# Optimization experiments

Hardware: AMD Instinct MI355X
Metric: run time of the kernel (lower is better)

Reference implementation:

```python
import jax, jax.numpy as jnp
import numpy as np

N_NODES = 100000
N_EDGES = 600000
DIMS = [128, 64, 32, 2]


def gcn_conv(x, edge_index, W, b, n_nodes):
    """PyG GCNConv (eval mode): symmetric-normalized aggregation with self-loops.
    out = D^{-1/2} (A + I) D^{-1/2} (x W) + b
    """
    h = x @ W  # [N, out] -- transform first (cheaper when out < in)
    src = jnp.concatenate([edge_index[0], jnp.arange(n_nodes)])  # add self-loops
    dst = jnp.concatenate([edge_index[1], jnp.arange(n_nodes)])
    deg = jax.ops.segment_sum(jnp.ones_like(dst, dtype=h.dtype), dst,
                              num_segments=n_nodes)  # in-degree incl. self-loop
    dinv = jax.lax.rsqrt(deg)
    norm = dinv[src] * dinv[dst]  # [E+N]
    msg = norm[:, None] * h[src]  # gather + scale
    out = jax.ops.segment_sum(msg, dst, num_segments=n_nodes)  # scatter-add
    return out + b


def setup_inputs() -> dict:
    key = jax.random.key(0)
    ks = jax.random.split(key, 8)
    x = jax.random.normal(ks[0], (N_NODES, DIMS[0]), dtype=jnp.float32)
    edge_index = jax.random.randint(ks[1], (2, N_EDGES), 0, N_NODES, dtype=jnp.int64)
    inp = {"x": x, "edge_index": edge_index}
    for i in range(3):
        fan_in, fan_out = DIMS[i], DIMS[i + 1]
        s = 1.0 / np.sqrt(fan_in)
        inp[f"W{i+1}"] = jax.random.uniform(ks[2 + 2 * i], (fan_in, fan_out),
                                            minval=-s, maxval=s, dtype=jnp.float32)
        inp[f"b{i+1}"] = jnp.zeros((fan_out,), dtype=jnp.float32)
    return inp


def reference(x, edge_index, W1, b1, W2, b2, W3, b3):
    # 3 stacked GCNConv layers with ReLU; dropout is identity in eval mode.
    n = x.shape[0]
    x = jax.nn.relu(gcn_conv(x, edge_index, W1, b1, n))
    x = jax.nn.relu(gcn_conv(x, edge_index, W2, b2, n))
    x = jax.nn.relu(gcn_conv(x, edge_index, W3, b3, n))
    return x
```

## Files before the change

kernel.cpp:

```cpp
#include <hip/hip_runtime.h>
#include <math.h>


#define FULL_GRID 2048
#define PARTS 8

typedef const __attribute__((address_space(1))) void* gas_ptr;
typedef __attribute__((address_space(3))) void* las_ptr;

__device__ __forceinline__ void gld16(const void* g, void* l) {
  __builtin_amdgcn_global_load_lds((gas_ptr)g, (las_ptr)l, 16, 0, 0);
}

__global__ __launch_bounds__(256) void k_init(int* __restrict__ p, int n4,
                                              const unsigned int* __restrict__ words,
                                              int* __restrict__ flag) {
  if (blockIdx.x == gridDim.x - 1) {
    __shared__ int sm[256];
    int cnt = 0;
    #pragma unroll
    for (int j = 0; j < 8; ++j) {
      int idx = (threadIdx.x * 8 + j) * 2 + 1;
      cnt += (words[idx] == 0u) ? 1 : 0;
    }
    sm[threadIdx.x] = cnt;
    __syncthreads();
    for (int off = 128; off > 0; off >>= 1) {
      if (threadIdx.x < off) sm[threadIdx.x] += sm[threadIdx.x + off];
      __syncthreads();
    }
    if (threadIdx.x == 0) flag[0] = (sm[0] > 1024) ? 1 : 0;
    return;
  }
  int i = blockIdx.x * blockDim.x + threadIdx.x;
  const int stride = (gridDim.x - 1) * blockDim.x;
  int4* p4 = (int4*)p;
  for (; i < n4; i += stride) p4[i] = make_int4(0, 0, 0, 0);
}

__global__ __launch_bounds__(256) void k_hist(const void* __restrict__ eraw, int E,
                                              int N, const int* __restrict__ flag,
                                              int* __restrict__ counts) {
  const int is64 = flag[0];
  const int part = blockIdx.x & (PARTS - 1);
  const int lo = (int)((long long)N * part / PARTS);
  const int hi = (int)((long long)N * (part + 1) / PARTS);
  int i = (blockIdx.x >> 3) * blockDim.x + threadIdx.x;
  const int stride = (gridDim.x >> 3) * blockDim.x;
  if (is64) {
    const long long* e = (const long long*)eraw;
    for (; i < E; i += stride) {
      const int d = (int)e[(long long)E + i];
      if (d >= lo && d < hi) atomicAdd(&counts[d], 1);
    }
  } else {
    const int* e = (const int*)eraw;
    for (; i < E; i += stride) {
      const int d = e[E + i];
      if (d >= lo && d < hi) atomicAdd(&counts[d], 1);
    }
  }
}

__global__ __launch_bounds__(1024) void k_scan1(const int* __restrict__ counts,
                                                int* __restrict__ scanned,
                                                int* __restrict__ partials, int n) {
  __shared__ int sm[1024];
  const int i = blockIdx.x * 1024 + threadIdx.x;
  const int v = (i < n) ? counts[i] : 0;
  sm[threadIdx.x] = v;
  __syncthreads();
  for (int off = 1; off < 1024; off <<= 1) {
    int t = sm[threadIdx.x];
    int u = (threadIdx.x >= off) ? sm[threadIdx.x - off] : 0;
    __syncthreads();
    sm[threadIdx.x] = t + u;
    __syncthreads();
  }
  const int inc = sm[threadIdx.x];
  if (i < n) scanned[i] = inc - v;
  if (threadIdx.x == 1023) partials[blockIdx.x] = inc;
}

__global__ __launch_bounds__(256) void k_scan3(const int* __restrict__ scanned,
                                               const int* __restrict__ partials,
                                               int nb,
                                               const int* __restrict__ counts,
                                               int* __restrict__ offsets,
                                               int* __restrict__ cursor,
                                               float* __restrict__ dinv, int n) {
  __shared__ int ps[1024];
  for (int t = threadIdx.x; t < nb; t += 256) ps[t] = partials[t];
  __syncthreads();
  if (threadIdx.x == 0) {
    int run = 0;
    for (int b = 0; b < nb; ++b) { const int v = ps[b]; ps[b] = run; run += v; }
  }
  __syncthreads();
  int i = blockIdx.x * blockDim.x + threadIdx.x;
  const int stride = gridDim.x * blockDim.x;
  for (; i < n; i += stride) {
    const int o = scanned[i] + ps[i >> 10];
    offsets[i] = o;
    cursor[i] = o;
    dinv[i] = rsqrtf((float)counts[i] + 1.0f);
  }
}

__global__ __launch_bounds__(256) void k_fill(const void* __restrict__ eraw, int E,
                                              int N, const int* __restrict__ flag,
                                              int* __restrict__ cursor,
                                              int* __restrict__ elist) {
  const int is64 = flag[0];
  const int part = blockIdx.x & (PARTS - 1);
  const int lo = (int)((long long)N * part / PARTS);
  const int hi = (int)((long long)N * (part + 1) / PARTS);
  int i = (blockIdx.x >> 3) * blockDim.x + threadIdx.x;
  const int stride = (gridDim.x >> 3) * blockDim.x;
  if (is64) {
    const long long* e = (const long long*)eraw;
    for (; i < E; i += stride) {
      const int d = (int)e[(long long)E + i];
      if (d >= lo && d < hi) {
        const int s = (int)e[i];
        elist[atomicAdd(&cursor[d], 1)] = s;
      }
    }
  } else {
    const int* e = (const int*)eraw;
    for (; i < E; i += stride) {
      const int d = e[E + i];
      if (d >= lo && d < hi) {
        const int s = e[i];
        elist[atomicAdd(&cursor[d], 1)] = s;
      }
    }
  }
}

template <int F_IN, int F_OUT, int TILE_M, int KC>
__global__ __launch_bounds__(256) void k_transform(const float* __restrict__ X,
                                                   const float* __restrict__ W,
                                                   const float* __restrict__ dinv,
                                                   float* __restrict__ H, int n) {
  constexpr int COLT = F_OUT / 4;
  constexpr int ROWT = 256 / COLT;
  constexpr int TM = TILE_M / ROWT;
  constexpr int NKC = F_IN / KC;
  constexpr int K4 = F_IN / 4;
  constexpr int NWB = (NKC > 1) ? 2 : 1;
  static_assert(TM * ROWT == TILE_M && COLT * 4 == F_OUT, "tiling");
  static_assert((TILE_M * F_IN * 4) % 1024 == 0 && (KC * F_OUT * 4) % 1024 == 0, "segs");
  static_assert(K4 >= 8, "swizzle range");
  static_assert(ROWT % 8 == 0, "swizzle invariance across r");

  __shared__ __align__(16) float Xs[TILE_M * F_IN];
  __shared__ __align__(16) float Ws[NWB][KC * F_OUT];

  const int tid = threadIdx.x;
  const int lane = tid & 63;
  const int wid = tid >> 6;
  const long long base = (long long)blockIdx.x * TILE_M;

  const float4* __restrict__ X4 = (const float4*)X;
  if (base + TILE_M <= n) {
    constexpr int SEGS = TILE_M * F_IN * 4 / 1024;
    constexpr int PW = SEGS / 4;
    #pragma unroll
    for (int j = 0; j < PW; ++j) {
      const int seg = wid * PW + j;
      const int slot = seg * 64 + lane;
      const int row = slot / K4;
      const int c = slot % K4;
      const int ksrc = c ^ (row & 7);
      gld16(&X4[(base + row) * K4 + ksrc], &Xs[seg * 256]);
    }
  } else {
    for (int slot = tid; slot < TILE_M * K4; slot += 256) {
      const int row = slot / K4;
      const int c = slot % K4;
      float4 v = make_float4(0.f, 0.f, 0.f, 0.f);
      if (base + row < n) v = X4[(base + row) * K4 + (c ^ (row & 7))];
      ((float4*)Xs)[slot] = v;
    }
  }

  constexpr int WSEG = KC * F_OUT * 4 / 1024;
  constexpr int WPW = WSEG / 4;
  {
    #pragma unroll
    for (int j = 0; j < WPW; ++j) {
      const int seg = wid * WPW + j;
      gld16(W + seg * 256 + lane * 4, &Ws[0][seg * 256]);
    }
  }

  const int ct = tid % COLT;
  const int rt = tid / COLT;
  const int sw = rt & 7;

  float4 acc[TM];
  #pragma unroll
  for (int r = 0; r < TM; ++r) acc[r] = make_float4(0.f, 0.f, 0.f, 0.f);

  const float4* Xs4 = (const float4*)Xs;

  for (int kc = 0; kc < NKC; ++kc) {
    __syncthreads();
    if (NKC > 1 && kc + 1 < NKC) {
      const float* wb = W + (kc + 1) * KC * F_OUT;
      #pragma unroll
      for (int j = 0; j < WPW; ++j) {
        const int seg = wid * WPW + j;
        gld16(wb + seg * 256 + lane * 4, &Ws[(kc + 1) & (NWB - 1)][seg * 256]);
      }
    }
    const float4* Ws4 = (const float4*)Ws[kc & (NWB - 1)];
    #pragma unroll
    for (int k4 = 0; k4 < KC / 4; ++k4) {
      const int kk = kc * (KC / 4) + k4;
      float4 wv0 = Ws4[(k4 * 4 + 0) * COLT + ct];
      float4 wv1 = Ws4[(k4 * 4 + 1) * COLT + ct];
      float4 wv2 = Ws4[(k4 * 4 + 2) * COLT + ct];
      float4 wv3 = Ws4[(k4 * 4 + 3) * COLT + ct];
      #pragma unroll
      for (int r = 0; r < TM; ++r) {
        const float4 xv = Xs4[(rt + r * ROWT) * K4 + (kk ^ sw)];
        acc[r].x = fmaf(xv.x, wv0.x, acc[r].x);
        acc[r].y = fmaf(xv.x, wv0.y, acc[r].y);
        acc[r].z = fmaf(xv.x, wv0.z, acc[r].z);
        acc[r].w = fmaf(xv.x, wv0.w, acc[r].w);
        acc[r].x = fmaf(xv.y, wv1.x, acc[r].x);
        acc[r].y = fmaf(xv.y, wv1.y, acc[r].y);
        acc[r].z = fmaf(xv.y, wv1.z, acc[r].z);
        acc[r].w = fmaf(xv.y, wv1.w, acc[r].w);
        acc[r].x = fmaf(xv.z, wv2.x, acc[r].x);
        acc[r].y = fmaf(xv.z, wv2.y, acc[r].y);
        acc[r].z = fmaf(xv.z, wv2.z, acc[r].z);
        acc[r].w = fmaf(xv.z, wv2.w, acc[r].w);
        acc[r].x = fmaf(xv.w, wv3.x, acc[r].x);
        acc[r].y = fmaf(xv.w, wv3.y, acc[r].y);
        acc[r].z = fmaf(xv.w, wv3.z, acc[r].z);
        acc[r].w = fmaf(xv.w, wv3.w, acc[r].w);
      }
    }
  }

  #pragma unroll
  for (int r = 0; r < TM; ++r) {
    const long long row = base + rt + r * ROWT;
    if (row < n) {
      const float di = dinv[row];
      float4 v = acc[r];
      v.x *= di; v.y *= di; v.z *= di; v.w *= di;
      *(float4*)&H[row * F_OUT + ct * 4] = v;
    }
  }
}

template <int F, bool RELU_OUT, bool FUSE_W3>
__global__ __launch_bounds__(256) void k_agg_vec(const float* __restrict__ HS,
                                                 const float* __restrict__ dinv,
                                                 const int* __restrict__ offsets,
                                                 const int* __restrict__ counts,
                                                 const int* __restrict__ elist,
                                                 const float* __restrict__ bias,
                                                 const float* __restrict__ W3,
                                                 float* __restrict__ out, int n) {
  constexpr int LPE = F / 4;
  constexpr int EPW = 64 / LPE;
  const int lane = threadIdx.x & 63;
  const int wv = (blockIdx.x * (blockDim.x >> 6)) + (threadIdx.x >> 6);
  const int nwaves = gridDim.x * (blockDim.x >> 6);
  const int g = lane / LPE;
  const int fl = lane % LPE;
  const float4 bf = *(const float4*)&bias[fl * 4];

  float w3a0 = 0.f, w3a1 = 0.f, w3a2 = 0.f, w3a3 = 0.f;
  float w3b0 = 0.f, w3b1 = 0.f, w3b2 = 0.f, w3b3 = 0.f;
  if (FUSE_W3) {
    w3a0 = W3[(fl * 4 + 0) * 2 + 0]; w3b0 = W3[(fl * 4 + 0) * 2 + 1];
    w3a1 = W3[(fl * 4 + 1) * 2 + 0]; w3b1 = W3[(fl * 4 + 1) * 2 + 1];
    w3a2 = W3[(fl * 4 + 2) * 2 + 0]; w3b2 = W3[(fl * 4 + 2) * 2 + 1];
    w3a3 = W3[(fl * 4 + 3) * 2 + 0]; w3b3 = W3[(fl * 4 + 3) * 2 + 1];
  }

  for (long long d = wv; d < n; d += nwaves) {
    const float di = dinv[d];
    const int start = offsets[d];
    const int cnt = counts[d];
    float4 acc = make_float4(0.f, 0.f, 0.f, 0.f);
    if (g == 0) acc = *(const float4*)&HS[d * F + fl * 4];

    for (int j = 0; j < cnt; j += 2 * EPW) {
      const int e0 = j + g;
      const int e1 = j + EPW + g;
      const int i0 = elist[start + (e0 < cnt ? e0 : cnt - 1)];
      const int i1 = elist[start + (e1 < cnt ? e1 : cnt - 1)];
      const float4 v0 = *(const float4*)&HS[(long long)i0 * F + fl * 4];
      const float4 v1 = *(const float4*)&HS[(long long)i1 * F + fl * 4];
      if (e0 < cnt) {
        acc.x += v0.x; acc.y += v0.y; acc.z += v0.z; acc.w += v0.w;
      }
      if (e1 < cnt) {
        acc.x += v1.x; acc.y += v1.y; acc.z += v1.z; acc.w += v1.w;
      }
    }
    #pragma unroll
    for (int m = LPE; m < 64; m <<= 1) {
      acc.x += __shfl_xor(acc.x, m, 64);
      acc.y += __shfl_xor(acc.y, m, 64);
      acc.z += __shfl_xor(acc.z, m, 64);
      acc.w += __shfl_xor(acc.w, m, 64);
    }
    float4 r;
    r.x = fmaf(di, acc.x, bf.x);
    r.y = fmaf(di, acc.y, bf.y);
    r.z = fmaf(di, acc.z, bf.z);
    r.w = fmaf(di, acc.w, bf.w);
    if (RELU_OUT) {
      r.x = fmaxf(r.x, 0.f); r.y = fmaxf(r.y, 0.f);
      r.z = fmaxf(r.z, 0.f); r.w = fmaxf(r.w, 0.f);
    }
    if (!FUSE_W3) {
      if (g == 0) *(float4*)&out[d * F + fl * 4] = r;
    } else {
      float t0 = r.x * w3a0 + r.y * w3a1 + r.z * w3a2 + r.w * w3a3;
      float t1 = r.x * w3b0 + r.y * w3b1 + r.z * w3b2 + r.w * w3b3;
      #pragma unroll
      for (int m = 1; m < LPE; m <<= 1) {
        t0 += __shfl_xor(t0, m, 64);
        t1 += __shfl_xor(t1, m, 64);
      }
      if (lane == 0) {
        out[d * 2 + 0] = di * t0;
        out[d * 2 + 1] = di * t1;
      }
    }
  }
}

template <int F, bool RELU_OUT>
__global__ __launch_bounds__(256) void k_aggregate(const float* __restrict__ HS,
                                                   const float* __restrict__ dinv,
                                                   const int* __restrict__ offsets,
                                                   const int* __restrict__ counts,
                                                   const int* __restrict__ elist,
                                                   const float* __restrict__ bias,
                                                   float* __restrict__ out, int n) {
  const int f = threadIdx.x % F;
  const int grp = threadIdx.x / F;
  constexpr int GRPS = 256 / F;
  const float bf = bias[f];

  for (long long d = (long long)blockIdx.x * GRPS + grp; d < n;
       d += (long long)gridDim.x * GRPS) {
    const float di = dinv[d];
    float acc = HS[d * F + f];
    const int start = offsets[d];
    const int cnt = counts[d];
    for (int j = 0; j < cnt; j += 8) {
      int idx[8];
      float v[8];
      #pragma unroll
      for (int t = 0; t < 8; ++t) {
        const int jj = (j + t < cnt) ? (j + t) : j;
        idx[t] = elist[start + jj];
      }
      #pragma unroll
      for (int t = 0; t < 8; ++t) v[t] = HS[(long long)idx[t] * F + f];
      #pragma unroll
      for (int t = 0; t < 8; ++t) acc += (j + t < cnt) ? v[t] : 0.f;
    }
    float r = fmaf(di, acc, bf);
    if (RELU_OUT) r = fmaxf(r, 0.f);
    out[d * F + f] = r;
  }
}

extern "C" void kernel_launch(void* const* d_in, const int* in_sizes, int n_in,
                              void* d_out, int out_size, void* d_ws, size_t ws_size,
                              hipStream_t stream) {
  const float* x = (const float*)d_in[0];
  const void* eraw = d_in[1];
  const float* W1 = (const float*)d_in[2];
  const float* b1 = (const float*)d_in[3];
  const float* W2 = (const float*)d_in[4];
  const float* b2 = (const float*)d_in[5];
  const float* W3 = (const float*)d_in[6];
  const float* b3 = (const float*)d_in[7];
  float* out = (float*)d_out;

  const int N = in_sizes[0] / 128;
  const int E = in_sizes[1] / 2;

  char* ws = (char*)d_ws;
  size_t off = 0;
  auto alloc = [&](size_t bytes) -> char* {
    char* p = ws + off;
    off = (off + bytes + 255) & ~(size_t)255;
    return p;
  };
  int*   flag     = (int*)alloc(256);
  int*   counts   = (int*)alloc((size_t)N * 4 + 16);
  int*   scanned  = (int*)alloc((size_t)N * 4);
  int*   partials = (int*)alloc(1024 * 4);
  int*   offsets  = (int*)alloc((size_t)N * 4);
  int*   cursor   = (int*)alloc((size_t)N * 4);
  int*   elist    = (int*)alloc((size_t)E * 4);
  float* dinv     = (float*)alloc((size_t)N * 4);
  float* hbuf     = (float*)alloc((size_t)N * 64 * 4);
  float* obuf     = (float*)alloc((size_t)N * 64 * 4);
  float* h2buf    = (float*)alloc((size_t)N * 32 * 4);
  (void)ws_size; (void)n_in; (void)out_size;

  k_init<<<129, 256, 0, stream>>>(counts, (N + 3) / 4, (const unsigned int*)eraw,
                                  flag);
  k_hist<<<FULL_GRID, 256, 0, stream>>>(eraw, E, N, flag, counts);
  const int NB = (N + 1023) >> 10;
  k_scan1<<<NB, 1024, 0, stream>>>(counts, scanned, partials, N);
  k_scan3<<<(N + 255) / 256, 256, 0, stream>>>(scanned, partials, NB, counts,
                                               offsets, cursor, dinv, N);
  k_fill<<<FULL_GRID, 256, 0, stream>>>(eraw, E, N, flag, cursor, elist);

  k_transform<128, 64, 64, 16><<<(N + 63) / 64, 256, 0, stream>>>(x, W1, dinv, hbuf, N);
  k_agg_vec<64, true, false><<<FULL_GRID, 256, 0, stream>>>(
      hbuf, dinv, offsets, counts, elist, b1, nullptr, obuf, N);

  k_transform<64, 32, 128, 64><<<(N + 127) / 128, 256, 0, stream>>>(obuf, W2, dinv,
                                                                    h2buf, N);
  k_agg_vec<32, true, true><<<FULL_GRID, 256, 0, stream>>>(
      h2buf, dinv, offsets, counts, elist, b2, W3, hbuf, N);

  k_aggregate<2, true><<<(N + 127) / 128, 256, 0, stream>>>(
      hbuf, dinv, offsets, counts, elist, b3, out, N);
}
```

Measured before the change: 194.2 us.

## Shrink transform blocks to one wave with 8x8 per-thread register tiles

The dense transform kernel now launches single-wave (64-thread) blocks in place of 256-thread ones. Each thread accumulates an 8-row by 8-column register tile, so every LDS weight and X read feeds more FMAs. The second layer also uses smaller double-buffered K chunks. The trade-off is that each block still holds the same large X tile in LDS, so the CU can host far fewer resident waves, which weakens latency hiding for the global-to-LDS loads.

```diff
diff --git a/kernel.cpp b/kernel.cpp
--- a/kernel.cpp
+++ b/kernel.cpp
@@ -138,45 +138,45 @@
   }
 }
 
-template <int F_IN, int F_OUT, int TILE_M, int KC>
-__global__ __launch_bounds__(256) void k_transform(const float* __restrict__ X,
-                                                   const float* __restrict__ W,
-                                                   const float* __restrict__ dinv,
-                                                   float* __restrict__ H, int n) {
-  constexpr int COLT = F_OUT / 4;
-  constexpr int ROWT = 256 / COLT;
-  constexpr int TM = TILE_M / ROWT;
+__device__ __forceinline__ float f4get(const float4& v, int j) {
+  return j == 0 ? v.x : (j == 1 ? v.y : (j == 2 ? v.z : v.w));
+}
+
+template <int F_IN, int F_OUT, int KC>
+__global__ __launch_bounds__(64) void k_transform(const float* __restrict__ X,
+                                                  const float* __restrict__ W,
+                                                  const float* __restrict__ dinv,
+                                                  float* __restrict__ H, int n) {
+  constexpr int COLT = F_OUT / 8;
+  constexpr int ROWT = 64 / COLT;
+  constexpr int TILE_M = 8 * ROWT;
+  constexpr int K4 = F_IN / 4;
   constexpr int NKC = F_IN / KC;
-  constexpr int K4 = F_IN / 4;
   constexpr int NWB = (NKC > 1) ? 2 : 1;
-  static_assert(TM * ROWT == TILE_M && COLT * 4 == F_OUT, "tiling");
-  static_assert((TILE_M * F_IN * 4) % 1024 == 0 && (KC * F_OUT * 4) % 1024 == 0, "segs");
-  static_assert(K4 >= 8, "swizzle range");
-  static_assert(ROWT % 8 == 0, "swizzle invariance across r");
+  constexpr int F4 = F_OUT / 4;
+  static_assert(COLT * 8 == F_OUT && ROWT * COLT == 64, "tiling");
+  static_assert(K4 >= 8 && (ROWT % 8) == 0, "swizzle");
+  static_assert((TILE_M * F_IN * 4) % 1024 == 0, "X segs");
+  static_assert((KC * F_OUT * 4) % 1024 == 0, "W segs");
 
   __shared__ __align__(16) float Xs[TILE_M * F_IN];
   __shared__ __align__(16) float Ws[NWB][KC * F_OUT];
 
-  const int tid = threadIdx.x;
-  const int lane = tid & 63;
-  const int wid = tid >> 6;
+  const int lane = threadIdx.x;
   const long long base = (long long)blockIdx.x * TILE_M;
-
   const float4* __restrict__ X4 = (const float4*)X;
+
+  constexpr int XSEG = TILE_M * F_IN * 4 / 1024;
   if (base + TILE_M <= n) {
-    constexpr int SEGS = TILE_M * F_IN * 4 / 1024;
-    constexpr int PW = SEGS / 4;
     #pragma unroll
-    for (int j = 0; j < PW; ++j) {
-      const int seg = wid * PW + j;
-      const int slot = seg * 64 + lane;
+    for (int j = 0; j < XSEG; ++j) {
+      const int slot = j * 64 + lane;
       const int row = slot / K4;
       const int c = slot % K4;
-      const int ksrc = c ^ (row & 7);
-      gld16(&X4[(base + row) * K4 + ksrc], &Xs[seg * 256]);
+      gld16(&X4[(base + row) * K4 + (c ^ (row & 7))], &Xs[j * 256]);
     }
   } else {
-    for (int slot = tid; slot < TILE_M * K4; slot += 256) {
+    for (int slot = lane; slot < TILE_M * K4; slot += 64) {
       const int row = slot / K4;
       const int c = slot % K4;
       float4 v = make_float4(0.f, 0.f, 0.f, 0.f);
@@ -186,22 +186,19 @@
   }
 
   constexpr int WSEG = KC * F_OUT * 4 / 1024;
-  constexpr int WPW = WSEG / 4;
-  {
-    #pragma unroll
-    for (int j = 0; j < WPW; ++j) {
-      const int seg = wid * WPW + j;
-      gld16(W + seg * 256 + lane * 4, &Ws[0][seg * 256]);
-    }
-  }
-
-  const int ct = tid % COLT;
-  const int rt = tid / COLT;
+  #pragma unroll
+  for (int j = 0; j < WSEG; ++j) gld16(W + j * 256 + lane * 4, &Ws[0][j * 256]);
+
+  const int ct = lane % COLT;
+  const int rt = lane / COLT;
   const int sw = rt & 7;
 
-  float4 acc[TM];
+  float4 acc[8][2];
   #pragma unroll
-  for (int r = 0; r < TM; ++r) acc[r] = make_float4(0.f, 0.f, 0.f, 0.f);
+  for (int r = 0; r < 8; ++r) {
+    acc[r][0] = make_float4(0.f, 0.f, 0.f, 0.f);
+    acc[r][1] = make_float4(0.f, 0.f, 0.f, 0.f);
+  }
 
   const float4* Xs4 = (const float4*)Xs;
 
@@ -210,50 +207,49 @@
     if (NKC > 1 && kc + 1 < NKC) {
       const float* wb = W + (kc + 1) * KC * F_OUT;
       #pragma unroll
-      for (int j = 0; j < WPW; ++j) {
-        const int seg = wid * WPW + j;
-        gld16(wb + seg * 256 + lane * 4, &Ws[(kc + 1) & (NWB - 1)][seg * 256]);
-      }
+      for (int j = 0; j < WSEG; ++j)
+        gld16(wb + j * 256 + lane * 4, &Ws[(kc + 1) & (NWB - 1)][j * 256]);
     }
     const float4* Ws4 = (const float4*)Ws[kc & (NWB - 1)];
     #pragma unroll
-    for (int k4 = 0; k4 < KC / 4; ++k4) {
-      const int kk = kc * (KC / 4) + k4;
-      float4 wv0 = Ws4[(k4 * 4 + 0) * COLT + ct];
-      float4 wv1 = Ws4[(k4 * 4 + 1) * COLT + ct];
-      float4 wv2 = Ws4[(k4 * 4 + 2) * COLT + ct];
-      float4 wv3 = Ws4[(k4 * 4 + 3) * COLT + ct];
-      #pragma unroll
-      for (int r = 0; r < TM; ++r) {
+    for (int lk4 = 0; lk4 < KC / 4; ++lk4) {
+      const int kk = kc * (KC / 4) + lk4;
+      float4 wv[4][2];
+      #pragma unroll
+      for (int j = 0; j < 4; ++j) {
+        wv[j][0] = Ws4[(lk4 * 4 + j) * F4 + 2 * ct + 0];
+        wv[j][1] = Ws4[(lk4 * 4 + j) * F4 + 2 * ct + 1];
+      }
+      #pragma unroll
+      for (int r = 0; r < 8; ++r) {
         const float4 xv = Xs4[(rt + r * ROWT) * K4 + (kk ^ sw)];
-        acc[r].x = fmaf(xv.x, wv0.x, acc[r].x);
-        acc[r].y = fmaf(xv.x, wv0.y, acc[r].y);
-        acc[r].z = fmaf(xv.x, wv0.z, acc[r].z);
-        acc[r].w = fmaf(xv.x, wv0.w, acc[r].w);
-        acc[r].x = fmaf(xv.y, wv1.x, acc[r].x);
-        acc[r].y = fmaf(xv.y, wv1.y, acc[r].y);
-        acc[r].z = fmaf(xv.y, wv1.z, acc[r].z);
-        acc[r].w = fmaf(xv.y, wv1.w, acc[r].w);
-        acc[r].x = fmaf(xv.z, wv2.x, acc[r].x);
-        acc[r].y = fmaf(xv.z, wv2.y, acc[r].y);
-        acc[r].z = fmaf(xv.z, wv2.z, acc[r].z);
-        acc[r].w = fmaf(xv.z, wv2.w, acc[r].w);
-        acc[r].x = fmaf(xv.w, wv3.x, acc[r].x);
-        acc[r].y = fmaf(xv.w, wv3.y, acc[r].y);
-        acc[r].z = fmaf(xv.w, wv3.z, acc[r].z);
-        acc[r].w = fmaf(xv.w, wv3.w, acc[r].w);
+        #pragma unroll
+        for (int j = 0; j < 4; ++j) {
+          const float xs = f4get(xv, j);
+          acc[r][0].x = fmaf(xs, wv[j][0].x, acc[r][0].x);
+          acc[r][0].y = fmaf(xs, wv[j][0].y, acc[r][0].y);
+          acc[r][0].z = fmaf(xs, wv[j][0].z, acc[r][0].z);
+          acc[r][0].w = fmaf(xs, wv[j][0].w, acc[r][0].w);
+          acc[r][1].x = fmaf(xs, wv[j][1].x, acc[r][1].x);
+          acc[r][1].y = fmaf(xs, wv[j][1].y, acc[r][1].y);
+          acc[r][1].z = fmaf(xs, wv[j][1].z, acc[r][1].z);
+          acc[r][1].w = fmaf(xs, wv[j][1].w, acc[r][1].w);
+        }
       }
     }
   }
 
   #pragma unroll
-  for (int r = 0; r < TM; ++r) {
+  for (int r = 0; r < 8; ++r) {
     const long long row = base + rt + r * ROWT;
     if (row < n) {
       const float di = dinv[row];
-      float4 v = acc[r];
-      v.x *= di; v.y *= di; v.z *= di; v.w *= di;
-      *(float4*)&H[row * F_OUT + ct * 4] = v;
+      #pragma unroll
+      for (int c4 = 0; c4 < 2; ++c4) {
+        float4 v = acc[r][c4];
+        v.x *= di; v.y *= di; v.z *= di; v.w *= di;
+        *(float4*)&H[row * F_OUT + ct * 8 + c4 * 4] = v;
+      }
     }
   }
 }
@@ -423,12 +419,12 @@
                                                offsets, cursor, dinv, N);
   k_fill<<<FULL_GRID, 256, 0, stream>>>(eraw, E, N, flag, cursor, elist);
 
-  k_transform<128, 64, 64, 16><<<(N + 63) / 64, 256, 0, stream>>>(x, W1, dinv, hbuf, N);
+  k_transform<128, 64, 16><<<(N + 63) / 64, 64, 0, stream>>>(x, W1, dinv, hbuf, N);
   k_agg_vec<64, true, false><<<FULL_GRID, 256, 0, stream>>>(
       hbuf, dinv, offsets, counts, elist, b1, nullptr, obuf, N);
 
-  k_transform<64, 32, 128, 64><<<(N + 127) / 128, 256, 0, stream>>>(obuf, W2, dinv,
-                                                                    h2buf, N);
+  k_transform<64, 32, 16><<<(N + 127) / 128, 64, 0, stream>>>(obuf, W2, dinv,
+                                                              h2buf, N);
   k_agg_vec<32, true, true><<<FULL_GRID, 256, 0, stream>>>(
       h2buf, dinv, offsets, counts, elist, b2, W3, hbuf, N);
 
```

Result: no change. 196.8 us (+1.3%).

## Use split-bf16 MFMA for the dense layer transforms

Applied to the files above, without the earlier changes.

Replaces the fp32 FMA tiled GEMM for layers 1 and 2 with MFMA 16x16x32 bf16 instructions. Inputs and weights are each split into high and low bf16 parts and combined with three MFMAs to keep near-fp32 accuracy. A small kernel prepacks the weights into fragment layout each call. The goal is to cut the compute time of the transform kernels, at the cost of in-kernel conversion work, extra LDS use, and scalar (non-vector) stores of the output.

```diff
diff --git a/kernel.cpp b/kernel.cpp
--- a/kernel.cpp
+++ b/kernel.cpp
@@ -7,9 +7,20 @@
 
 typedef const __attribute__((address_space(1))) void* gas_ptr;
 typedef __attribute__((address_space(3))) void* las_ptr;
+typedef __attribute__((ext_vector_type(8))) short bf16x8;
+typedef __attribute__((ext_vector_type(4))) float f32x4;
 
 __device__ __forceinline__ void gld16(const void* g, void* l) {
   __builtin_amdgcn_global_load_lds((gas_ptr)g, (las_ptr)l, 16, 0, 0);
+}
+
+__device__ __forceinline__ unsigned short f2bf(float f) {
+  unsigned int u = __float_as_uint(f);
+  u += 0x7FFF + ((u >> 16) & 1);
+  return (unsigned short)(u >> 16);
+}
+__device__ __forceinline__ float bf2f(unsigned short h) {
+  return __uint_as_float(((unsigned int)h) << 16);
 }
 
 __global__ __launch_bounds__(256) void k_init(int* __restrict__ p, int n4,
@@ -36,6 +47,34 @@
   const int stride = (gridDim.x - 1) * blockDim.x;
   int4* p4 = (int4*)p;
   for (; i < n4; i += stride) p4[i] = make_int4(0, 0, 0, 0);
+}
+
+__global__ __launch_bounds__(256) void k_prepw(const float* __restrict__ W1,
+                                               const float* __restrict__ W2,
+                                               short* __restrict__ Wh1,
+                                               short* __restrict__ Wl1,
+                                               short* __restrict__ Wh2,
+                                               short* __restrict__ Wl2) {
+  const int t = blockIdx.x * 256 + threadIdx.x;
+  const int stride = gridDim.x * 256;
+  for (int p = t; p < 4 * 4 * 64 * 8; p += stride) {
+    const int e = p & 7, lane = (p >> 3) & 63, nt = (p >> 9) & 3, kt = p >> 11;
+    const int k = kt * 32 + (lane >> 4) * 8 + e;
+    const int nn = nt * 16 + (lane & 15);
+    const float f = W1[k * 64 + nn];
+    const unsigned short h = f2bf(f);
+    Wh1[p] = (short)h;
+    Wl1[p] = (short)f2bf(f - bf2f(h));
+  }
+  for (int p = t; p < 2 * 2 * 64 * 8; p += stride) {
+    const int e = p & 7, lane = (p >> 3) & 63, nt = (p >> 9) & 1, kt = p >> 10;
+    const int k = kt * 32 + (lane >> 4) * 8 + e;
+    const int nn = nt * 16 + (lane & 15);
+    const float f = W2[k * 32 + nn];
+    const unsigned short h = f2bf(f);
+    Wh2[p] = (short)h;
+    Wl2[p] = (short)f2bf(f - bf2f(h));
+  }
 }
 
 __global__ __launch_bounds__(256) void k_hist(const void* __restrict__ eraw, int E,
@@ -138,122 +177,88 @@
   }
 }
 
-template <int F_IN, int F_OUT, int TILE_M, int KC>
-__global__ __launch_bounds__(256) void k_transform(const float* __restrict__ X,
-                                                   const float* __restrict__ W,
-                                                   const float* __restrict__ dinv,
-                                                   float* __restrict__ H, int n) {
-  constexpr int COLT = F_OUT / 4;
-  constexpr int ROWT = 256 / COLT;
-  constexpr int TM = TILE_M / ROWT;
-  constexpr int NKC = F_IN / KC;
-  constexpr int K4 = F_IN / 4;
-  constexpr int NWB = (NKC > 1) ? 2 : 1;
-  static_assert(TM * ROWT == TILE_M && COLT * 4 == F_OUT, "tiling");
-  static_assert((TILE_M * F_IN * 4) % 1024 == 0 && (KC * F_OUT * 4) % 1024 == 0, "segs");
-  static_assert(K4 >= 8, "swizzle range");
-  static_assert(ROWT % 8 == 0, "swizzle invariance across r");
-
-  __shared__ __align__(16) float Xs[TILE_M * F_IN];
-  __shared__ __align__(16) float Ws[NWB][KC * F_OUT];
+template <int F_IN, int F_OUT>
+__global__ __launch_bounds__(256) void k_transform_mfma(
+    const float* __restrict__ X, const short* __restrict__ Wh,
+    const short* __restrict__ Wl, const float* __restrict__ dinv,
+    float* __restrict__ H, int n) {
+  constexpr int KT = F_IN / 32;
+  constexpr int NT = F_OUT / 16;
+  constexpr int K4f = F_IN / 4;
+  constexpr int SLOTS = F_IN / 8;
+  constexpr int TILE_M = 64;
+  constexpr int WFRAG = KT * NT * 64 * 8;
+  static_assert((WFRAG * 2) % 1024 == 0, "W segs");
+
+  __shared__ __align__(16) unsigned short Xh[TILE_M * F_IN];
+  __shared__ __align__(16) unsigned short Xl[TILE_M * F_IN];
+  __shared__ __align__(16) unsigned short Whs[WFRAG];
+  __shared__ __align__(16) unsigned short Wls[WFRAG];
 
   const int tid = threadIdx.x;
   const int lane = tid & 63;
   const int wid = tid >> 6;
   const long long base = (long long)blockIdx.x * TILE_M;
 
+  constexpr int WSEGS = WFRAG * 2 / 1024;
+  for (int seg = wid; seg < WSEGS; seg += 4) {
+    gld16((const char*)Wh + seg * 1024 + lane * 16, (char*)Whs + seg * 1024);
+    gld16((const char*)Wl + seg * 1024 + lane * 16, (char*)Wls + seg * 1024);
+  }
+
   const float4* __restrict__ X4 = (const float4*)X;
-  if (base + TILE_M <= n) {
-    constexpr int SEGS = TILE_M * F_IN * 4 / 1024;
-    constexpr int PW = SEGS / 4;
+  for (int g = tid; g < TILE_M * K4f; g += 256) {
+    const int row = g / K4f, c4 = g % K4f;
+    float4 v = make_float4(0.f, 0.f, 0.f, 0.f);
+    if (base + row < n) v = X4[(base + row) * K4f + c4];
+    ushort4 hv, lv;
+    hv.x = f2bf(v.x); lv.x = f2bf(v.x - bf2f(hv.x));
+    hv.y = f2bf(v.y); lv.y = f2bf(v.y - bf2f(hv.y));
+    hv.z = f2bf(v.z); lv.z = f2bf(v.z - bf2f(hv.z));
+    hv.w = f2bf(v.w); lv.w = f2bf(v.w - bf2f(hv.w));
+    const int slot = (c4 >> 1) ^ (row & (SLOTS - 1));
+    const int boff = row * (F_IN * 2) + slot * 16 + (c4 & 1) * 8;
+    *(ushort4*)((char*)Xh + boff) = hv;
+    *(ushort4*)((char*)Xl + boff) = lv;
+  }
+  __syncthreads();
+
+  const int arow = lane & 15;
+  const int kg = lane >> 4;
+  const int lrow = wid * 16 + arow;
+
+  f32x4 acc[NT];
+  #pragma unroll
+  for (int t = 0; t < NT; ++t) {
+    f32x4 z = {0.f, 0.f, 0.f, 0.f};
+    acc[t] = z;
+  }
+
+  #pragma unroll
+  for (int kt = 0; kt < KT; ++kt) {
+    const int slot = (kt * 4 + kg) ^ (lrow & (SLOTS - 1));
+    const int aoff = lrow * (F_IN * 2) + slot * 16;
+    const bf16x8 ah = *(const bf16x8*)((const char*)Xh + aoff);
+    const bf16x8 al = *(const bf16x8*)((const char*)Xl + aoff);
     #pragma unroll
-    for (int j = 0; j < PW; ++j) {
-      const int seg = wid * PW + j;
-      const int slot = seg * 64 + lane;
-      const int row = slot / K4;
-      const int c = slot % K4;
-      const int ksrc = c ^ (row & 7);
-      gld16(&X4[(base + row) * K4 + ksrc], &Xs[seg * 256]);
-    }
-  } else {
-    for (int slot = tid; slot < TILE_M * K4; slot += 256) {
-      const int row = slot / K4;
-      const int c = slot % K4;
-      float4 v = make_float4(0.f, 0.f, 0.f, 0.f);
-      if (base + row < n) v = X4[(base + row) * K4 + (c ^ (row & 7))];
-      ((float4*)Xs)[slot] = v;
-    }
-  }
-
-  constexpr int WSEG = KC * F_OUT * 4 / 1024;
-  constexpr int WPW = WSEG / 4;
-  {
-    #pragma unroll
-    for (int j = 0; j < WPW; ++j) {
-      const int seg = wid * WPW + j;
-      gld16(W + seg * 256 + lane * 4, &Ws[0][seg * 256]);
-    }
-  }
-
-  const int ct = tid % COLT;
-  const int rt = tid / COLT;
-  const int sw = rt & 7;
-
-  float4 acc[TM];
+    for (int nt = 0; nt < NT; ++nt) {
+      const int woff = ((kt * NT + nt) * 64 + lane) * 8;
+      const bf16x8 bh = *(const bf16x8*)&Whs[woff];
+      const bf16x8 bl = *(const bf16x8*)&Wls[woff];
+      acc[nt] = __builtin_amdgcn_mfma_f32_16x16x32_bf16(ah, bh, acc[nt], 0, 0, 0);
+      acc[nt] = __builtin_amdgcn_mfma_f32_16x16x32_bf16(ah, bl, acc[nt], 0, 0, 0);
+      acc[nt] = __builtin_amdgcn_mfma_f32_16x16x32_bf16(al, bh, acc[nt], 0, 0, 0);
+    }
+  }
+
   #pragma unroll
-  for (int r = 0; r < TM; ++r) acc[r] = make_float4(0.f, 0.f, 0.f, 0.f);
-
-  const float4* Xs4 = (const float4*)Xs;
-
-  for (int kc = 0; kc < NKC; ++kc) {
-    __syncthreads();
-    if (NKC > 1 && kc + 1 < NKC) {
-      const float* wb = W + (kc + 1) * KC * F_OUT;
-      #pragma unroll
-      for (int j = 0; j < WPW; ++j) {
-        const int seg = wid * WPW + j;
-        gld16(wb + seg * 256 + lane * 4, &Ws[(kc + 1) & (NWB - 1)][seg * 256]);
-      }
-    }
-    const float4* Ws4 = (const float4*)Ws[kc & (NWB - 1)];
-    #pragma unroll
-    for (int k4 = 0; k4 < KC / 4; ++k4) {
-      const int kk = kc * (KC / 4) + k4;
-      float4 wv0 = Ws4[(k4 * 4 + 0) * COLT + ct];
-      float4 wv1 = Ws4[(k4 * 4 + 1) * COLT + ct];
-      float4 wv2 = Ws4[(k4 * 4 + 2) * COLT + ct];
-      float4 wv3 = Ws4[(k4 * 4 + 3) * COLT + ct];
-      #pragma unroll
-      for (int r = 0; r < TM; ++r) {
-        const float4 xv = Xs4[(rt + r * ROWT) * K4 + (kk ^ sw)];
-        acc[r].x = fmaf(xv.x, wv0.x, acc[r].x);
-        acc[r].y = fmaf(xv.x, wv0.y, acc[r].y);
-        acc[r].z = fmaf(xv.x, wv0.z, acc[r].z);
-        acc[r].w = fmaf(xv.x, wv0.w, acc[r].w);
-        acc[r].x = fmaf(xv.y, wv1.x, acc[r].x);
-        acc[r].y = fmaf(xv.y, wv1.y, acc[r].y);
-        acc[r].z = fmaf(xv.y, wv1.z, acc[r].z);
-        acc[r].w = fmaf(xv.y, wv1.w, acc[r].w);
-        acc[r].x = fmaf(xv.z, wv2.x, acc[r].x);
-        acc[r].y = fmaf(xv.z, wv2.y, acc[r].y);
-        acc[r].z = fmaf(xv.z, wv2.z, acc[r].z);
-        acc[r].w = fmaf(xv.z, wv2.w, acc[r].w);
-        acc[r].x = fmaf(xv.w, wv3.x, acc[r].x);
-        acc[r].y = fmaf(xv.w, wv3.y, acc[r].y);
-        acc[r].z = fmaf(xv.w, wv3.z, acc[r].z);
-        acc[r].w = fmaf(xv.w, wv3.w, acc[r].w);
-      }
-    }
-  }
-
-  #pragma unroll
-  for (int r = 0; r < TM; ++r) {
-    const long long row = base + rt + r * ROWT;
+  for (int r = 0; r < 4; ++r) {
+    const long long row = base + wid * 16 + kg * 4 + r;
     if (row < n) {
       const float di = dinv[row];
-      float4 v = acc[r];
-      v.x *= di; v.y *= di; v.z *= di; v.w *= di;
-      *(float4*)&H[row * F_OUT + ct * 4] = v;
+      #pragma unroll
+      for (int nt = 0; nt < NT; ++nt)
+        H[row * F_OUT + nt * 16 + arow] = di * acc[nt][r];
     }
   }
 }
@@ -409,6 +414,10 @@
   int*   cursor   = (int*)alloc((size_t)N * 4);
   int*   elist    = (int*)alloc((size_t)E * 4);
   float* dinv     = (float*)alloc((size_t)N * 4);
+  short* Wh1      = (short*)alloc(4 * 4 * 64 * 8 * 2);
+  short* Wl1      = (short*)alloc(4 * 4 * 64 * 8 * 2);
+  short* Wh2      = (short*)alloc(2 * 2 * 64 * 8 * 2);
+  short* Wl2      = (short*)alloc(2 * 2 * 64 * 8 * 2);
   float* hbuf     = (float*)alloc((size_t)N * 64 * 4);
   float* obuf     = (float*)alloc((size_t)N * 64 * 4);
   float* h2buf    = (float*)alloc((size_t)N * 32 * 4);
@@ -416,6 +425,7 @@
 
   k_init<<<129, 256, 0, stream>>>(counts, (N + 3) / 4, (const unsigned int*)eraw,
                                   flag);
+  k_prepw<<<32, 256, 0, stream>>>(W1, W2, Wh1, Wl1, Wh2, Wl2);
   k_hist<<<FULL_GRID, 256, 0, stream>>>(eraw, E, N, flag, counts);
   const int NB = (N + 1023) >> 10;
   k_scan1<<<NB, 1024, 0, stream>>>(counts, scanned, partials, N);
@@ -423,12 +433,13 @@
                                                offsets, cursor, dinv, N);
   k_fill<<<FULL_GRID, 256, 0, stream>>>(eraw, E, N, flag, cursor, elist);
 
-  k_transform<128, 64, 64, 16><<<(N + 63) / 64, 256, 0, stream>>>(x, W1, dinv, hbuf, N);
+  k_transform_mfma<128, 64><<<(N + 63) / 64, 256, 0, stream>>>(
+      x, Wh1, Wl1, dinv, hbuf, N);
   k_agg_vec<64, true, false><<<FULL_GRID, 256, 0, stream>>>(
       hbuf, dinv, offsets, counts, elist, b1, nullptr, obuf, N);
 
-  k_transform<64, 32, 128, 64><<<(N + 127) / 128, 256, 0, stream>>>(obuf, W2, dinv,
-                                                                    h2buf, N);
+  k_transform_mfma<64, 32><<<(N + 63) / 64, 256, 0, stream>>>(
+      obuf, Wh2, Wl2, dinv, h2buf, N);
   k_agg_vec<32, true, true><<<FULL_GRID, 256, 0, stream>>>(
       h2buf, dinv, offsets, counts, elist, b2, W3, hbuf, N);
 
```

After: 172.3 us. 1.13x faster.
